# Optimization experiments

Hardware: AMD Instinct MI355X
Metric: run time of the kernel (lower is better)

## Reference

```python
import jax, jax.numpy as jnp
import numpy as np

EMB = 1024
HID = 1536
NE = 8


def setup_inputs() -> dict:
    key = jax.random.key(0)
    ks = jax.random.split(key, 8)
    B, N, E, H, ne = 4, 2048, EMB, HID, NE
    s = 1.0 / np.sqrt(E)
    sh = 1.0 / np.sqrt(H)
    return {
        "x": jax.random.normal(ks[0], (B, N, E), dtype=jnp.float32),
        "Wr": jax.random.uniform(ks[1], (E, ne), minval=-s, maxval=s, dtype=jnp.float32),
        "br": jax.random.uniform(ks[2], (ne,), minval=-s, maxval=s, dtype=jnp.float32),
        "W1": jax.random.uniform(ks[3], (ne, E, H), minval=-s, maxval=s, dtype=jnp.float32),
        "b1": jax.random.uniform(ks[4], (ne, H), minval=-s, maxval=s, dtype=jnp.float32),
        "W2": jax.random.uniform(ks[5], (ne, H, E), minval=-sh, maxval=sh, dtype=jnp.float32),
        "b2": jax.random.uniform(ks[6], (ne, E), minval=-sh, maxval=sh, dtype=jnp.float32),
        "k": 2,
    }


def reference(x, Wr, br, W1, b1, W2, b2, k):
    B, N, E = x.shape
    T = B * N
    ne = Wr.shape[1]
    flat = x.reshape(T, E)
    logits = flat @ Wr + br                      # [T, ne]
    _, topk_idx = jax.lax.top_k(logits, k)       # [T, k]
    # counts[t, e] = number of top-k slots of token t assigned to expert e
    counts = jax.nn.one_hot(topk_idx, ne, dtype=flat.dtype).sum(axis=1)  # [T, ne]
    out = jnp.zeros_like(flat)
    for e in range(ne):  # small fixed loop over experts (structurally distinct weights)
        h = jax.nn.gelu(flat @ W1[e] + b1[e], approximate=False)  # torch nn.GELU = exact erf
        y = h @ W2[e] + b2[e]
        out = out + counts[:, e:e + 1] * y
    out = out / k
    return out.reshape(B, N, E)
```

## Files before the change

### kernel.cpp

```cpp
#include <hip/hip_runtime.h>
#include <hip/hip_bf16.h>
#include <math.h>

#define T_TOK 8192
#define EMB   1024
#define HID   1536
#define NE    8

typedef float  floatx4 __attribute__((ext_vector_type(4)));
typedef __bf16 bf16x8  __attribute__((ext_vector_type(8)));

#define WS_COUNTS   0
#define WS_OFFSETS  1024
#define WS_FLAGS    2048
#define WS_TOKMAP   8192
#define WS_TOKLIST  270336
#define WS_YBUF     532480
#define WS_W1T      34086912
#define WS_W2T      59252736
#define WS_H        84418560
#define WS_NEEDED   135143424

__device__ __forceinline__ float eload(const void* p, size_t idx, bool f32) {
  return f32 ? ((const float*)p)[idx] : (float)(((const __bf16*)p)[idx]);
}

__device__ __forceinline__ void glds16(const void* g, void* l) {
  __builtin_amdgcn_global_load_lds(
      (const __attribute__((address_space(1))) unsigned int*)g,
      (__attribute__((address_space(3))) unsigned int*)l, 16, 0, 0);
}

__global__ __launch_bounds__(256)
void sniff_kernel(const void* p0, const void* p1, const void* p2, const void* p3,
                  const void* p4, const void* p5, const void* p6, int* flags) {
  const void* ps[7] = {p0, p1, p2, p3, p4, p5, p6};
  const int nelem[7] = {T_TOK * EMB, EMB * NE, NE, NE * EMB * HID, NE * HID, NE * HID * EMB, NE * EMB};
  int t = blockIdx.x;
  const unsigned* w = (const unsigned*)ps[t];
  int nw = nelem[t] / 2;
  if (nw > 2048) nw = 2048;
  __shared__ int s_pl, s_nz;
  if (threadIdx.x == 0) { s_pl = 0; s_nz = 0; }
  __syncthreads();
  int pl = 0, nz = 0;
  for (int i = threadIdx.x; i < nw; i += 256) {
    unsigned v = w[i];
    if (v == 0) continue;
    nz++;
    unsigned e = (v >> 23) & 0xFF;
    if (e >= 100 && e <= 150) pl++;
  }
  atomicAdd(&s_pl, pl);
  atomicAdd(&s_nz, nz);
  __syncthreads();
  if (threadIdx.x == 0) flags[t] = (2 * s_pl > s_nz) ? 1 : 0;
}

__global__ __launch_bounds__(256)
void prep_kernel(const void* __restrict__ W1, const void* __restrict__ W2,
                 __bf16* __restrict__ w1t, __bf16* __restrict__ w2t,
                 const void* __restrict__ x, const void* __restrict__ Wr,
                 const void* __restrict__ br, const int* __restrict__ kptr,
                 const int* __restrict__ flags, int* __restrict__ topk,
                 __bf16* __restrict__ xbf) {
  const int bid = blockIdx.x;
  const int tid = threadIdx.x;
  const int wave = tid >> 6;
  const int lane = tid & 63;

  if (bid < 1536) {
    const void* in; __bf16* out; int K, N; bool f32; int t;
    if (bid < 768) {
      in = W1; out = w1t; K = EMB; N = HID; f32 = flags[3] != 0;
      t = bid * 4 + wave;
    } else {
      in = W2; out = w2t; K = HID; N = EMB; f32 = flags[5] != 0;
      t = (bid - 768) * 4 + wave;
    }
    const int ntile = N / 64;
    const int e  = t / (384);
    const int r  = t % 384;
    const int kb = r / ntile;
    const int nb = r % ntile;
    const size_t eoff = (size_t)e * (size_t)K * (size_t)N;
    const int k0 = kb * 64 + (lane >> 3) * 8;
    const int n0 = nb * 64 + (lane & 7) * 8;

    if (f32) {
      floatx4 a0[8], a1[8];
#pragma unroll
      for (int i = 0; i < 8; ++i) {
        const float* g = (const float*)in + eoff + (size_t)(k0 + i) * N + n0;
        a0[i] = *(const floatx4*)g;
        a1[i] = *(const floatx4*)(g + 4);
      }
#pragma unroll
      for (int j = 0; j < 8; ++j) {
        bf16x8 o;
#pragma unroll
        for (int i = 0; i < 8; ++i)
          o[i] = (__bf16)(j < 4 ? a0[i][j] : a1[i][j - 4]);
        *(bf16x8*)(out + eoff + (size_t)(n0 + j) * K + k0) = o;
      }
    } else {
      bf16x8 a[8];
#pragma unroll
      for (int i = 0; i < 8; ++i)
        a[i] = *(const bf16x8*)((const __bf16*)in + eoff + (size_t)(k0 + i) * N + n0);
#pragma unroll
      for (int j = 0; j < 8; ++j) {
        bf16x8 o;
#pragma unroll
        for (int i = 0; i < 8; ++i) o[i] = a[i][j];
        *(bf16x8*)(out + eoff + (size_t)(n0 + j) * K + k0) = o;
      }
    }
    return;
  }

  const bool xf32  = flags[0] != 0;
  const bool wrf32 = flags[1] != 0;
  const bool brf32 = flags[2] != 0;
  const int t = (bid - 1536) * 4 + wave;

  float xv[16];
  {
    size_t base = (size_t)t * EMB + lane * 16;
    if (xf32) {
      const float* g = (const float*)x + base;
#pragma unroll
      for (int c = 0; c < 4; ++c) {
        float4 v = *(const float4*)(g + c * 4);
        xv[c * 4 + 0] = v.x; xv[c * 4 + 1] = v.y; xv[c * 4 + 2] = v.z; xv[c * 4 + 3] = v.w;
      }
    } else {
      bf16x8 u = *(const bf16x8*)((const __bf16*)x + base);
      bf16x8 v = *(const bf16x8*)((const __bf16*)x + base + 8);
#pragma unroll
      for (int j = 0; j < 8; ++j) { xv[j] = (float)u[j]; xv[8 + j] = (float)v[j]; }
    }
  }
  {
    bf16x8 o0, o1;
#pragma unroll
    for (int j = 0; j < 8; ++j) { o0[j] = (__bf16)xv[j]; o1[j] = (__bf16)xv[8 + j]; }
    __bf16* xo = xbf + (size_t)t * EMB + lane * 16;
    *(bf16x8*)xo = o0;
    *(bf16x8*)(xo + 8) = o1;
  }
  float acc[NE];
#pragma unroll
  for (int e = 0; e < NE; ++e) acc[e] = 0.f;
  if (wrf32) {
#pragma unroll
    for (int j = 0; j < 16; ++j) {
      const float* wr = (const float*)Wr + (size_t)(lane * 16 + j) * NE;
#pragma unroll
      for (int e = 0; e < NE; ++e) acc[e] += xv[j] * wr[e];
    }
  } else {
#pragma unroll
    for (int j = 0; j < 16; ++j) {
      bf16x8 wr = *(const bf16x8*)((const __bf16*)Wr + (size_t)(lane * 16 + j) * NE);
#pragma unroll
      for (int e = 0; e < NE; ++e) acc[e] += xv[j] * (float)wr[e];
    }
  }
#pragma unroll
  for (int e = 0; e < NE; ++e) {
#pragma unroll
    for (int off = 32; off > 0; off >>= 1)
      acc[e] += __shfl_xor(acc[e], off, 64);
  }
  if (lane == 0) {
    int k = kptr[0];
    if (k < 1) k = 1; if (k > NE) k = NE;
    float lg[NE];
#pragma unroll
    for (int e = 0; e < NE; ++e) lg[e] = acc[e] + eload(br, e, brf32);
    for (int s = 0; s < k; ++s) {
      int bi = 0; float bv = lg[0];
#pragma unroll
      for (int e = 1; e < NE; ++e) { if (lg[e] > bv) { bv = lg[e]; bi = e; } }
      lg[bi] = -3.0e38f;
      topk[t * 8 + s] = bi;
    }
  }
}

__global__ __launch_bounds__(1024)
void bin_kernel(const int* __restrict__ kptr, int* __restrict__ tokmap,
                int* __restrict__ tok_list, int* __restrict__ counts,
                int* __restrict__ offsets) {
  __shared__ int lcnt[NE];
  __shared__ int soff[NE + 1];
  const int tid = threadIdx.x;
  if (tid < NE) lcnt[tid] = 0;
  __syncthreads();
  int k = kptr[0];
  if (k < 1) k = 1; if (k > NE) k = NE;
  for (int t = tid; t < T_TOK; t += 1024) {
    for (int s = 0; s < k; ++s) {
      int e = tokmap[t * 8 + s] & 7;
      int pos = atomicAdd(&lcnt[e], 1);
      tok_list[e * T_TOK + pos] = t;
      tokmap[t * 8 + s] = (e << 16) | pos;
    }
  }
  __syncthreads();
  if (tid == 0) {
    int s = 0;
    for (int e = 0; e < NE; ++e) { soff[e] = s; s += lcnt[e]; }
    soff[NE] = s;
  }
  __syncthreads();
  if (tid < NE) counts[tid] = lcnt[tid];
  if (tid <= NE) offsets[tid] = soff[tid];
  for (int e = 0; e < NE; ++e) {
    const int c = lcnt[e];
    const int end = (c + 127) & ~127;
    for (int i = c + tid; i < end; i += 1024) tok_list[e * T_TOK + i] = 0;
  }
}


__global__ __launch_bounds__(256, 4)
void gemm1_kernel(const __bf16* __restrict__ xbf, const __bf16* __restrict__ w1t,
                  const void* __restrict__ b1, const int* __restrict__ counts,
                  const int* __restrict__ offsets, const int* __restrict__ tok_list,
                  const int* __restrict__ flags, __bf16* __restrict__ hbuf) {
  const int flat = blockIdx.x;
  const int e   = flat & 7;
  const int idx = flat >> 3;
  const int g   = idx / 12;
  const int nT  = idx % 12;
  const int cnt = counts[e];
  const bool b1f32 = flags[4] != 0;

  __shared__ __align__(16) __bf16 As[128 * 64];
  __shared__ __align__(16) __bf16 Bs[128 * 64];

  const int wave = threadIdx.x >> 6;
  const int lane = threadIdx.x & 63;
  const int lrow = lane >> 3;
  const int cgs  = (lane & 7) ^ lrow;

  int Rst[4];
#pragma unroll
  for (int q = 0; q < 4; ++q) Rst[q] = (q * 4 + wave) * 8 + lrow;

  const __bf16* pB[4];
#pragma unroll
  for (int q = 0; q < 4; ++q)
    pB[q] = w1t + ((size_t)e * HID + nT * 128 + Rst[q]) * EMB + cgs * 8;

  const int wm = (wave & 1) * 64;
  const int wn = (wave >> 1) * 64;
  const int fr = lane & 15;
  const int fc = lane >> 4;
  int aOff0[4], aOff1[4], bOff0[4], bOff1[4];
#pragma unroll
  for (int i = 0; i < 4; ++i) {
    int R = wm + i * 16 + fr;
    aOff0[i] = R * 128 + (((fc)     ^ (R & 7)) << 4);
    aOff1[i] = R * 128 + (((fc + 4) ^ (R & 7)) << 4);
  }
#pragma unroll
  for (int j = 0; j < 4; ++j) {
    int R = wn + j * 16 + fr;
    bOff0[j] = R * 128 + (((fc)     ^ (R & 7)) << 4);
    bOff1[j] = R * 128 + (((fc + 4) ^ (R & 7)) << 4);
  }

  const int colBase = nT * 128 + wn + fr;
  float bv[4];
#pragma unroll
  for (int j = 0; j < 4; ++j) bv[j] = eload(b1, (size_t)e * HID + colBase + j * 16, b1f32);

  for (int mT = g; mT * 128 < cnt; mT += 16) {
    const __bf16* pA[4];
#pragma unroll
    for (int q = 0; q < 4; ++q) {
      const int tok = tok_list[e * T_TOK + mT * 128 + Rst[q]];
      pA[q] = xbf + (size_t)tok * EMB + cgs * 8;
    }

    floatx4 acc[4][4];
#pragma unroll
    for (int i = 0; i < 4; ++i)
#pragma unroll
      for (int j = 0; j < 4; ++j) acc[i][j] = (floatx4){0.f, 0.f, 0.f, 0.f};

    for (int kb = 0; kb < EMB / 64; ++kb) {
      __syncthreads();
#pragma unroll
      for (int q = 0; q < 4; ++q) glds16(pA[q] + (size_t)kb * 64, As + (q * 4 + wave) * 512);
#pragma unroll
      for (int q = 0; q < 4; ++q) glds16(pB[q] + (size_t)kb * 64, Bs + (q * 4 + wave) * 512);
      __syncthreads();
      bf16x8 af[4], bfr[4];
#pragma unroll
      for (int i = 0; i < 4; ++i) af[i]  = *(const bf16x8*)((const char*)As + aOff0[i]);
#pragma unroll
      for (int j = 0; j < 4; ++j) bfr[j] = *(const bf16x8*)((const char*)Bs + bOff0[j]);
#pragma unroll
      for (int i = 0; i < 4; ++i)
#pragma unroll
        for (int j = 0; j < 4; ++j)
          acc[i][j] = __builtin_amdgcn_mfma_f32_16x16x32_bf16(af[i], bfr[j], acc[i][j], 0, 0, 0);
#pragma unroll
      for (int i = 0; i < 4; ++i) af[i]  = *(const bf16x8*)((const char*)As + aOff1[i]);
#pragma unroll
      for (int j = 0; j < 4; ++j) bfr[j] = *(const bf16x8*)((const char*)Bs + bOff1[j]);
#pragma unroll
      for (int i = 0; i < 4; ++i)
#pragma unroll
        for (int j = 0; j < 4; ++j)
          acc[i][j] = __builtin_amdgcn_mfma_f32_16x16x32_bf16(af[i], bfr[j], acc[i][j], 0, 0, 0);
    }

    const int hBase = offsets[e] + mT * 128;
#pragma unroll
    for (int i = 0; i < 4; ++i) {
      const int rowLoc = wm + i * 16 + fc * 4;
#pragma unroll
      for (int r = 0; r < 4; ++r) {
        const int row = rowLoc + r;
        if (mT * 128 + row < cnt) {
          __bf16* hp = hbuf + (size_t)(hBase + row) * HID + colBase;
#pragma unroll
          for (int j = 0; j < 4; ++j) {
            float v = acc[i][j][r] + bv[j];
            float gl = 0.5f * v * (1.0f + erff(v * 0.70710678118654752f));
            hp[j * 16] = (__bf16)gl;
          }
        }
      }
    }
  }
}

__global__ __launch_bounds__(256, 4)
void gemm2_kernel(const __bf16* __restrict__ hbuf, const __bf16* __restrict__ w2t,
                  const void* __restrict__ b2, const int* __restrict__ counts,
                  const int* __restrict__ offsets, const int* __restrict__ flags,
                  __bf16* __restrict__ ybuf) {
  const int flat = blockIdx.x;
  const int e   = flat & 7;
  const int idx = flat >> 3;
  const int g   = idx >> 3;
  const int nT  = idx & 7;
  const int cnt = counts[e];
  const bool b2f32 = flags[6] != 0;

  __shared__ __align__(16) __bf16 As[128 * 64];
  __shared__ __align__(16) __bf16 Bs[128 * 64];

  const int wave = threadIdx.x >> 6;
  const int lane = threadIdx.x & 63;
  const int lrow = lane >> 3;
  const int cgs  = (lane & 7) ^ lrow;

  int Rst[4];
#pragma unroll
  for (int q = 0; q < 4; ++q) Rst[q] = (q * 4 + wave) * 8 + lrow;

  const __bf16* pB[4];
#pragma unroll
  for (int q = 0; q < 4; ++q)
    pB[q] = w2t + ((size_t)e * EMB + nT * 128 + Rst[q]) * HID + cgs * 8;

  const int wm = (wave & 1) * 64;
  const int wn = (wave >> 1) * 64;
  const int fr = lane & 15;
  const int fc = lane >> 4;
  int aOff0[4], aOff1[4], bOff0[4], bOff1[4];
#pragma unroll
  for (int i = 0; i < 4; ++i) {
    int R = wm + i * 16 + fr;
    aOff0[i] = R * 128 + (((fc)     ^ (R & 7)) << 4);
    aOff1[i] = R * 128 + (((fc + 4) ^ (R & 7)) << 4);
  }
#pragma unroll
  for (int j = 0; j < 4; ++j) {
    int R = wn + j * 16 + fr;
    bOff0[j] = R * 128 + (((fc)     ^ (R & 7)) << 4);
    bOff1[j] = R * 128 + (((fc + 4) ^ (R & 7)) << 4);
  }

  const int colBase = nT * 128 + wn + fr;
  float bv[4];
#pragma unroll
  for (int j = 0; j < 4; ++j) bv[j] = eload(b2, (size_t)e * EMB + colBase + j * 16, b2f32);

  for (int mT = g; mT * 128 < cnt; mT += 16) {
    const int rowBase = offsets[e] + mT * 128;
    const __bf16* pA[4];
#pragma unroll
    for (int q = 0; q < 4; ++q)
      pA[q] = hbuf + (size_t)(rowBase + Rst[q]) * HID + cgs * 8;

    floatx4 acc[4][4];
#pragma unroll
    for (int i = 0; i < 4; ++i)
#pragma unroll
      for (int j = 0; j < 4; ++j) acc[i][j] = (floatx4){0.f, 0.f, 0.f, 0.f};

    for (int kb = 0; kb < HID / 64; ++kb) {
      __syncthreads();
#pragma unroll
      for (int q = 0; q < 4; ++q) glds16(pA[q] + (size_t)kb * 64, As + (q * 4 + wave) * 512);
#pragma unroll
      for (int q = 0; q < 4; ++q) glds16(pB[q] + (size_t)kb * 64, Bs + (q * 4 + wave) * 512);
      __syncthreads();
      bf16x8 af[4], bfr[4];
#pragma unroll
      for (int i = 0; i < 4; ++i) af[i]  = *(const bf16x8*)((const char*)As + aOff0[i]);
#pragma unroll
      for (int j = 0; j < 4; ++j) bfr[j] = *(const bf16x8*)((const char*)Bs + bOff0[j]);
#pragma unroll
      for (int i = 0; i < 4; ++i)
#pragma unroll
        for (int j = 0; j < 4; ++j)
          acc[i][j] = __builtin_amdgcn_mfma_f32_16x16x32_bf16(af[i], bfr[j], acc[i][j], 0, 0, 0);
#pragma unroll
      for (int i = 0; i < 4; ++i) af[i]  = *(const bf16x8*)((const char*)As + aOff1[i]);
#pragma unroll
      for (int j = 0; j < 4; ++j) bfr[j] = *(const bf16x8*)((const char*)Bs + bOff1[j]);
#pragma unroll
      for (int i = 0; i < 4; ++i)
#pragma unroll
        for (int j = 0; j < 4; ++j)
          acc[i][j] = __builtin_amdgcn_mfma_f32_16x16x32_bf16(af[i], bfr[j], acc[i][j], 0, 0, 0);
    }

#pragma unroll
    for (int i = 0; i < 4; ++i) {
      const int rowLoc = wm + i * 16 + fc * 4;
#pragma unroll
      for (int r = 0; r < 4; ++r) {
        const int row = rowLoc + r;
        if (mT * 128 + row < cnt) {
          __bf16* yp = ybuf + (size_t)(rowBase + row) * EMB + colBase;
#pragma unroll
          for (int j = 0; j < 4; ++j)
            yp[j * 16] = (__bf16)(acc[i][j][r] + bv[j]);
        }
      }
    }
  }
}

__global__ __launch_bounds__(256)
void combine_kernel(const __bf16* __restrict__ ybuf, const int* __restrict__ tokmap,
                    const int* __restrict__ offsets, const int* __restrict__ kptr,
                    const int* __restrict__ flags, void* __restrict__ out) {
  const bool f32 = flags[0] != 0;
  const int wave = threadIdx.x >> 6;
  const int lane = threadIdx.x & 63;
  const int t = blockIdx.x * 4 + wave;
  int k = kptr[0];
  if (k < 1) k = 1; if (k > NE) k = NE;
  const float invk = 1.0f / (float)k;
  int rows[NE];
  for (int s = 0; s < k; ++s) {
    int m = tokmap[t * 8 + s];
    rows[s] = offsets[(m >> 16) & 7] + (m & 0xFFFF);
  }
#pragma unroll
  for (int c = 0; c < 2; ++c) {
    const int i = c * 512 + lane * 8;
    float a[8];
#pragma unroll
    for (int j = 0; j < 8; ++j) a[j] = 0.f;
    for (int s = 0; s < k; ++s) {
      bf16x8 y = *(const bf16x8*)(ybuf + (size_t)rows[s] * EMB + i);
#pragma unroll
      for (int j = 0; j < 8; ++j) a[j] += (float)y[j];
    }
    if (f32) {
      float* op = (float*)out + (size_t)t * EMB + i;
      float4 u = {a[0] * invk, a[1] * invk, a[2] * invk, a[3] * invk};
      float4 v = {a[4] * invk, a[5] * invk, a[6] * invk, a[7] * invk};
      *(float4*)op = u;
      *(float4*)(op + 4) = v;
    } else {
      bf16x8 o;
#pragma unroll
      for (int j = 0; j < 8; ++j) o[j] = (__bf16)(a[j] * invk);
      *(bf16x8*)((__bf16*)out + (size_t)t * EMB + i) = o;
    }
  }
}

extern "C" void kernel_launch(void* const* d_in, const int* in_sizes, int n_in,
                              void* d_out, int out_size, void* d_ws, size_t ws_size,
                              hipStream_t stream) {
  (void)in_sizes; (void)n_in; (void)out_size;
  if (ws_size < (size_t)WS_NEEDED) return;

  const void* x  = d_in[0];
  const void* Wr = d_in[1];
  const void* br = d_in[2];
  const void* W1 = d_in[3];
  const void* b1 = d_in[4];
  const void* W2 = d_in[5];
  const void* b2 = d_in[6];
  const int* kptr = (const int*)d_in[7];

  char* ws = (char*)d_ws;
  int*    counts   = (int*)(ws + WS_COUNTS);
  int*    offsets  = (int*)(ws + WS_OFFSETS);
  int*    flags    = (int*)(ws + WS_FLAGS);
  int*    tokmap   = (int*)(ws + WS_TOKMAP);
  int*    tok_list = (int*)(ws + WS_TOKLIST);
  __bf16* ybuf     = (__bf16*)(ws + WS_YBUF);
  __bf16* xbf      = (__bf16*)(ws + WS_YBUF);
  __bf16* w1t      = (__bf16*)(ws + WS_W1T);
  __bf16* w2t      = (__bf16*)(ws + WS_W2T);
  __bf16* hbuf     = (__bf16*)(ws + WS_H);

  sniff_kernel<<<dim3(7), 256, 0, stream>>>(x, Wr, br, W1, b1, W2, b2, flags);

  prep_kernel<<<dim3(1536 + T_TOK / 4), 256, 0, stream>>>(
      W1, W2, w1t, w2t, x, Wr, br, kptr, flags, tokmap, xbf);

  bin_kernel<<<dim3(1), 1024, 0, stream>>>(kptr, tokmap, tok_list, counts, offsets);

  gemm1_kernel<<<dim3(8 * 16 * 12), 256, 0, stream>>>(
      xbf, w1t, b1, counts, offsets, tok_list, flags, hbuf);
  gemm2_kernel<<<dim3(8 * 16 * 8), 256, 0, stream>>>(
      hbuf, w2t, b2, counts, offsets, flags, ybuf);

  combine_kernel<<<dim3(T_TOK / 4), 256, 0, stream>>>(ybuf, tokmap, offsets, kptr, flags, d_out);
}
```

Before: 385.0 us.

## Fuse dtype sniffing and token binning into prep, drop separate launches

Removes the separate sniff kernel and the single-block bin kernel. Each wave now sniffs input dtypes itself, and tokens are binned with global atomics directly in prep's top-k step. Expert offsets are recomputed from counts in each consumer, and gemm1 clamps the row index instead of relying on zero-padded token lists. This cuts two launches and a serial single-block pass. In exchange it adds redundant per-wave sniff loads, global atomic contention, a memset, and a nondeterministic row order within each expert.

```diff
diff --git a/kernel.cpp b/kernel.cpp
--- a/kernel.cpp
+++ b/kernel.cpp
@@ -11,8 +11,6 @@
 typedef __bf16 bf16x8  __attribute__((ext_vector_type(8)));
 
 #define WS_COUNTS   0
-#define WS_OFFSETS  1024
-#define WS_FLAGS    2048
 #define WS_TOKMAP   8192
 #define WS_TOKLIST  270336
 #define WS_YBUF     532480
@@ -21,6 +19,20 @@
 #define WS_H        84418560
 #define WS_NEEDED   135143424
 
+__device__ __forceinline__ bool wave_sniff_f32(const void* p, int nelem) {
+  const unsigned* w = (const unsigned*)p;
+  int nw = nelem >> 1; if (nw > 256) nw = 256;
+  const int lane = threadIdx.x & 63;
+  int pl = 0, nz = 0;
+  for (int i = lane; i < nw; i += 64) {
+    unsigned v = w[i];
+    if (v) { nz++; unsigned ex = (v >> 23) & 255; if (ex >= 100 && ex <= 150) pl++; }
+  }
+#pragma unroll
+  for (int off = 32; off; off >>= 1) { pl += __shfl_xor(pl, off, 64); nz += __shfl_xor(nz, off, 64); }
+  return 2 * pl > nz;
+}
+
 __device__ __forceinline__ float eload(const void* p, size_t idx, bool f32) {
   return f32 ? ((const float*)p)[idx] : (float)(((const __bf16*)p)[idx]);
 }
@@ -29,32 +41,6 @@
   __builtin_amdgcn_global_load_lds(
       (const __attribute__((address_space(1))) unsigned int*)g,
       (__attribute__((address_space(3))) unsigned int*)l, 16, 0, 0);
-}
-
-__global__ __launch_bounds__(256)
-void sniff_kernel(const void* p0, const void* p1, const void* p2, const void* p3,
-                  const void* p4, const void* p5, const void* p6, int* flags) {
-  const void* ps[7] = {p0, p1, p2, p3, p4, p5, p6};
-  const int nelem[7] = {T_TOK * EMB, EMB * NE, NE, NE * EMB * HID, NE * HID, NE * HID * EMB, NE * EMB};
-  int t = blockIdx.x;
-  const unsigned* w = (const unsigned*)ps[t];
-  int nw = nelem[t] / 2;
-  if (nw > 2048) nw = 2048;
-  __shared__ int s_pl, s_nz;
-  if (threadIdx.x == 0) { s_pl = 0; s_nz = 0; }
-  __syncthreads();
-  int pl = 0, nz = 0;
-  for (int i = threadIdx.x; i < nw; i += 256) {
-    unsigned v = w[i];
-    if (v == 0) continue;
-    nz++;
-    unsigned e = (v >> 23) & 0xFF;
-    if (e >= 100 && e <= 150) pl++;
-  }
-  atomicAdd(&s_pl, pl);
-  atomicAdd(&s_nz, nz);
-  __syncthreads();
-  if (threadIdx.x == 0) flags[t] = (2 * s_pl > s_nz) ? 1 : 0;
 }
 
 __global__ __launch_bounds__(256)
@@ -62,24 +48,25 @@
                  __bf16* __restrict__ w1t, __bf16* __restrict__ w2t,
                  const void* __restrict__ x, const void* __restrict__ Wr,
                  const void* __restrict__ br, const int* __restrict__ kptr,
-                 const int* __restrict__ flags, int* __restrict__ topk,
-                 __bf16* __restrict__ xbf) {
+                 int* __restrict__ tokmap, int* __restrict__ tok_list,
+                 int* __restrict__ counts, __bf16* __restrict__ xbf) {
   const int bid = blockIdx.x;
   const int tid = threadIdx.x;
   const int wave = tid >> 6;
   const int lane = tid & 63;
 
   if (bid < 1536) {
-    const void* in; __bf16* out; int K, N; bool f32; int t;
+    const void* in; __bf16* out; int K, N; int t;
     if (bid < 768) {
-      in = W1; out = w1t; K = EMB; N = HID; f32 = flags[3] != 0;
+      in = W1; out = w1t; K = EMB; N = HID;
       t = bid * 4 + wave;
     } else {
-      in = W2; out = w2t; K = HID; N = EMB; f32 = flags[5] != 0;
+      in = W2; out = w2t; K = HID; N = EMB;
       t = (bid - 768) * 4 + wave;
     }
+    const bool f32 = wave_sniff_f32(in, NE * EMB * HID);
     const int ntile = N / 64;
-    const int e  = t / (384);
+    const int e  = t / 384;
     const int r  = t % 384;
     const int kb = r / ntile;
     const int nb = r % ntile;
@@ -119,9 +106,9 @@
     return;
   }
 
-  const bool xf32  = flags[0] != 0;
-  const bool wrf32 = flags[1] != 0;
-  const bool brf32 = flags[2] != 0;
+  const bool xf32  = wave_sniff_f32(x, T_TOK * EMB);
+  const bool wrf32 = wave_sniff_f32(Wr, EMB * NE);
+  const bool brf32 = wave_sniff_f32(br, NE);
   const int t = (bid - 1536) * 4 + wave;
 
   float xv[16];
@@ -184,43 +171,10 @@
 #pragma unroll
       for (int e = 1; e < NE; ++e) { if (lg[e] > bv) { bv = lg[e]; bi = e; } }
       lg[bi] = -3.0e38f;
-      topk[t * 8 + s] = bi;
-    }
-  }
-}
-
-__global__ __launch_bounds__(1024)
-void bin_kernel(const int* __restrict__ kptr, int* __restrict__ tokmap,
-                int* __restrict__ tok_list, int* __restrict__ counts,
-                int* __restrict__ offsets) {
-  __shared__ int lcnt[NE];
-  __shared__ int soff[NE + 1];
-  const int tid = threadIdx.x;
-  if (tid < NE) lcnt[tid] = 0;
-  __syncthreads();
-  int k = kptr[0];
-  if (k < 1) k = 1; if (k > NE) k = NE;
-  for (int t = tid; t < T_TOK; t += 1024) {
-    for (int s = 0; s < k; ++s) {
-      int e = tokmap[t * 8 + s] & 7;
-      int pos = atomicAdd(&lcnt[e], 1);
-      tok_list[e * T_TOK + pos] = t;
-      tokmap[t * 8 + s] = (e << 16) | pos;
-    }
-  }
-  __syncthreads();
-  if (tid == 0) {
-    int s = 0;
-    for (int e = 0; e < NE; ++e) { soff[e] = s; s += lcnt[e]; }
-    soff[NE] = s;
-  }
-  __syncthreads();
-  if (tid < NE) counts[tid] = lcnt[tid];
-  if (tid <= NE) offsets[tid] = soff[tid];
-  for (int e = 0; e < NE; ++e) {
-    const int c = lcnt[e];
-    const int end = (c + 127) & ~127;
-    for (int i = c + tid; i < end; i += 1024) tok_list[e * T_TOK + i] = 0;
+      int pos = atomicAdd(&counts[bi], 1);
+      tok_list[bi * T_TOK + pos] = t;
+      tokmap[t * 8 + s] = (bi << 16) | pos;
+    }
   }
 }
 
@@ -228,15 +182,16 @@
 __global__ __launch_bounds__(256, 4)
 void gemm1_kernel(const __bf16* __restrict__ xbf, const __bf16* __restrict__ w1t,
                   const void* __restrict__ b1, const int* __restrict__ counts,
-                  const int* __restrict__ offsets, const int* __restrict__ tok_list,
-                  const int* __restrict__ flags, __bf16* __restrict__ hbuf) {
+                  const int* __restrict__ tok_list, __bf16* __restrict__ hbuf) {
   const int flat = blockIdx.x;
   const int e   = flat & 7;
   const int idx = flat >> 3;
   const int g   = idx / 12;
   const int nT  = idx % 12;
-  const int cnt = counts[e];
-  const bool b1f32 = flags[4] != 0;
+  int cnt = 0, off_e = 0;
+#pragma unroll
+  for (int i = 0; i < NE; ++i) { int c = counts[i]; if (i < e) off_e += c; if (i == e) cnt = c; }
+  const bool b1f32 = wave_sniff_f32(b1, NE * HID);
 
   __shared__ __align__(16) __bf16 As[128 * 64];
   __shared__ __align__(16) __bf16 Bs[128 * 64];
@@ -282,7 +237,9 @@
     const __bf16* pA[4];
 #pragma unroll
     for (int q = 0; q < 4; ++q) {
-      const int tok = tok_list[e * T_TOK + mT * 128 + Rst[q]];
+      int idxr = mT * 128 + Rst[q];
+      if (idxr > cnt - 1) idxr = cnt - 1;
+      const int tok = tok_list[e * T_TOK + idxr];
       pA[q] = xbf + (size_t)tok * EMB + cgs * 8;
     }
 
@@ -320,7 +277,7 @@
           acc[i][j] = __builtin_amdgcn_mfma_f32_16x16x32_bf16(af[i], bfr[j], acc[i][j], 0, 0, 0);
     }
 
-    const int hBase = offsets[e] + mT * 128;
+    const int hBase = off_e + mT * 128;
 #pragma unroll
     for (int i = 0; i < 4; ++i) {
       const int rowLoc = wm + i * 16 + fc * 4;
@@ -344,15 +301,16 @@
 __global__ __launch_bounds__(256, 4)
 void gemm2_kernel(const __bf16* __restrict__ hbuf, const __bf16* __restrict__ w2t,
                   const void* __restrict__ b2, const int* __restrict__ counts,
-                  const int* __restrict__ offsets, const int* __restrict__ flags,
                   __bf16* __restrict__ ybuf) {
   const int flat = blockIdx.x;
   const int e   = flat & 7;
   const int idx = flat >> 3;
   const int g   = idx >> 3;
   const int nT  = idx & 7;
-  const int cnt = counts[e];
-  const bool b2f32 = flags[6] != 0;
+  int cnt = 0, off_e = 0;
+#pragma unroll
+  for (int i = 0; i < NE; ++i) { int c = counts[i]; if (i < e) off_e += c; if (i == e) cnt = c; }
+  const bool b2f32 = wave_sniff_f32(b2, NE * EMB);
 
   __shared__ __align__(16) __bf16 As[128 * 64];
   __shared__ __align__(16) __bf16 Bs[128 * 64];
@@ -395,7 +353,7 @@
   for (int j = 0; j < 4; ++j) bv[j] = eload(b2, (size_t)e * EMB + colBase + j * 16, b2f32);
 
   for (int mT = g; mT * 128 < cnt; mT += 16) {
-    const int rowBase = offsets[e] + mT * 128;
+    const int rowBase = off_e + mT * 128;
     const __bf16* pA[4];
 #pragma unroll
     for (int q = 0; q < 4; ++q)
@@ -454,19 +412,26 @@
 
 __global__ __launch_bounds__(256)
 void combine_kernel(const __bf16* __restrict__ ybuf, const int* __restrict__ tokmap,
-                    const int* __restrict__ offsets, const int* __restrict__ kptr,
-                    const int* __restrict__ flags, void* __restrict__ out) {
-  const bool f32 = flags[0] != 0;
+                    const int* __restrict__ counts, const int* __restrict__ kptr,
+                    const void* __restrict__ x, void* __restrict__ out) {
+  const bool f32 = wave_sniff_f32(x, T_TOK * EMB);
   const int wave = threadIdx.x >> 6;
   const int lane = threadIdx.x & 63;
   const int t = blockIdx.x * 4 + wave;
   int k = kptr[0];
   if (k < 1) k = 1; if (k > NE) k = NE;
   const float invk = 1.0f / (float)k;
+  int cArr[NE];
+#pragma unroll
+  for (int i = 0; i < NE; ++i) cArr[i] = counts[i];
   int rows[NE];
   for (int s = 0; s < k; ++s) {
     int m = tokmap[t * 8 + s];
-    rows[s] = offsets[(m >> 16) & 7] + (m & 0xFFFF);
+    int es = (m >> 16) & 7;
+    int off = 0;
+#pragma unroll
+    for (int i = 0; i < NE; ++i) if (i < es) off += cArr[i];
+    rows[s] = off + (m & 0xFFFF);
   }
 #pragma unroll
   for (int c = 0; c < 2; ++c) {
@@ -511,8 +476,6 @@
 
   char* ws = (char*)d_ws;
   int*    counts   = (int*)(ws + WS_COUNTS);
-  int*    offsets  = (int*)(ws + WS_OFFSETS);
-  int*    flags    = (int*)(ws + WS_FLAGS);
   int*    tokmap   = (int*)(ws + WS_TOKMAP);
   int*    tok_list = (int*)(ws + WS_TOKLIST);
   __bf16* ybuf     = (__bf16*)(ws + WS_YBUF);
@@ -521,17 +484,15 @@
   __bf16* w2t      = (__bf16*)(ws + WS_W2T);
   __bf16* hbuf     = (__bf16*)(ws + WS_H);
 
-  sniff_kernel<<<dim3(7), 256, 0, stream>>>(x, Wr, br, W1, b1, W2, b2, flags);
+  hipMemsetAsync(counts, 0, NE * sizeof(int), stream);
 
   prep_kernel<<<dim3(1536 + T_TOK / 4), 256, 0, stream>>>(
-      W1, W2, w1t, w2t, x, Wr, br, kptr, flags, tokmap, xbf);
-
-  bin_kernel<<<dim3(1), 1024, 0, stream>>>(kptr, tokmap, tok_list, counts, offsets);
+      W1, W2, w1t, w2t, x, Wr, br, kptr, tokmap, tok_list, counts, xbf);
 
   gemm1_kernel<<<dim3(8 * 16 * 12), 256, 0, stream>>>(
-      xbf, w1t, b1, counts, offsets, tok_list, flags, hbuf);
+      xbf, w1t, b1, counts, tok_list, hbuf);
   gemm2_kernel<<<dim3(8 * 16 * 8), 256, 0, stream>>>(
-      hbuf, w2t, b2, counts, offsets, flags, ybuf);
-
-  combine_kernel<<<dim3(T_TOK / 4), 256, 0, stream>>>(ybuf, tokmap, offsets, kptr, flags, d_out);
-}
+      hbuf, w2t, b2, counts, ybuf);
+
+  combine_kernel<<<dim3(T_TOK / 4), 256, 0, stream>>>(ybuf, tokmap, counts, kptr, x, d_out);
+}
```

Result: slower. 511.9 us (+32.9%).
